# Optimization experiments

Measured on AMD Instinct MI355X. Metric: run time of the kernel, lower is better.

The kernel has to match this reference:

```python
import jax, jax.numpy as jnp
import numpy as np

NUM_NODES = 1_000_000
EMBED_DIM = 128
BATCH = 16384
K = 32  # max neighbors per node (padded)


def setup_inputs() -> dict:
    key = jax.random.key(0)
    k1, k2, k3, k4, k5, k6 = jax.random.split(key, 6)
    node_parameters = jax.random.normal(k1, (NUM_NODES, EMBED_DIM), dtype=jnp.float32) * 0.1
    node_indices = jax.random.randint(k2, (BATCH,), 0, NUM_NODES)
    pos_idx = jax.random.randint(k3, (BATCH, K), 0, NUM_NODES)
    pos_len = jax.random.randint(k4, (BATCH,), 0, K + 1)
    neg_idx = jax.random.randint(k5, (BATCH, K), 0, NUM_NODES)
    neg_len = jax.random.randint(k6, (BATCH,), 0, K + 1)
    return {
        "node_parameters": node_parameters,
        "node_indices": node_indices,
        "pos_idx": pos_idx,
        "pos_len": pos_len,
        "neg_idx": neg_idx,
        "neg_len": neg_len,
    }


def _masked_mean(table, idx, length):
    # table: [N, D], idx: [B, K], length: [B] -> [B, D]
    gathered = table[idx]  # [B, K, D]
    mask = (jnp.arange(idx.shape[1])[None, :] < length[:, None]).astype(table.dtype)  # [B, K]
    summed = jnp.einsum("bkd,bk->bd", gathered, mask)
    denom = length.astype(table.dtype)
    inv = jnp.where(denom > 0, 1.0 / jnp.maximum(denom, 1.0), 0.0)  # empty list -> zeros
    return summed * inv[:, None]


def reference(node_parameters, node_indices, pos_idx, pos_len, neg_idx, neg_len):
    node_embeds = node_parameters[node_indices]  # [B, D]
    pos_embeds = _masked_mean(node_parameters, pos_idx, pos_len)  # [B, D]
    neg_embeds = _masked_mean(node_parameters, neg_idx, neg_len)  # [B, D]
    return node_embeds, pos_embeds, neg_embeds
```

## Files before the change

### kernel.cpp

```cpp
#include <hip/hip_runtime.h>


constexpr int B = 16384;
constexpr int K = 32;

__global__ __launch_bounds__(256) void isne_kernel(
    const float* __restrict__ table,
    const int*   __restrict__ node_idx,
    const int*   __restrict__ pos_idx,
    const int*   __restrict__ pos_len,
    const int*   __restrict__ neg_idx,
    const int*   __restrict__ neg_len,
    float*       __restrict__ out)
{
    const int b     = blockIdx.x;
    const int tid   = threadIdx.x;
    const int side  = tid >> 7;
    const int stid  = tid & 127;
    const int grp   = stid >> 5;
    const int lane4 = stid & 31;
    const int sub   = stid >> 6;
    const int kbase = grp * 8;

    const float4* t4   = reinterpret_cast<const float4*>(table);
    float4*       out4 = reinterpret_cast<float4*>(out);

    if (tid < 32) {
        const int ni = node_idx[b];
        out4[(size_t)b * 32 + tid] = t4[(size_t)ni * 32 + tid];
    }

    const int* idxp = side ? neg_idx : pos_idx;
    const int  len  = (side ? neg_len : pos_len)[b];

    int ridx[8];
#pragma unroll
    for (int j = 0; j < 8; ++j) {
        const int k  = kbase + j;
        const int kk = (k < len) ? k : 0;
        ridx[j] = idxp[b * K + kk];
    }

    float4 v[8];
#pragma unroll
    for (int j = 0; j < 8; ++j) {
        v[j] = t4[(size_t)ridx[j] * 32 + lane4];
    }

    float4 acc = make_float4(0.f, 0.f, 0.f, 0.f);
#pragma unroll
    for (int j = 0; j < 8; ++j) {
        const float w = ((kbase + j) < len) ? 1.0f : 0.0f;
        acc.x += v[j].x * w;
        acc.y += v[j].y * w;
        acc.z += v[j].z * w;
        acc.w += v[j].w * w;
    }

    acc.x += __shfl_xor(acc.x, 32);
    acc.y += __shfl_xor(acc.y, 32);
    acc.z += __shfl_xor(acc.z, 32);
    acc.w += __shfl_xor(acc.w, 32);

    __shared__ float4 smem[2][32];
    if (sub == 1 && (stid & 63) < 32) smem[side][lane4] = acc;
    __syncthreads();
    if (sub == 0 && stid < 32) {
        float4 o = smem[side][lane4];
        o.x += acc.x; o.y += acc.y; o.z += acc.z; o.w += acc.w;
        const float inv = (len > 0) ? (1.0f / (float)len) : 0.0f;
        o.x *= inv; o.y *= inv; o.z *= inv; o.w *= inv;
        out4[((size_t)(1 + side) * B + b) * 32 + lane4] = o;
    }
}

extern "C" void kernel_launch(void* const* d_in, const int* in_sizes, int n_in,
                              void* d_out, int out_size, void* d_ws, size_t ws_size,
                              hipStream_t stream)
{
    const float* table    = (const float*)d_in[0];
    const int*   node_idx = (const int*)d_in[1];
    const int*   pos_idx  = (const int*)d_in[2];
    const int*   pos_len  = (const int*)d_in[3];
    const int*   neg_idx  = (const int*)d_in[4];
    const int*   neg_len  = (const int*)d_in[5];
    float*       out      = (float*)d_out;

    isne_kernel<<<B, 256, 0, stream>>>(table, node_idx, pos_idx, pos_len,
                                       neg_idx, neg_len, out);
}
```

Baseline: 609.3 us.

## Map one wave per batch row and side, skip gathers beyond list length

Restructures the kernel so each 64-lane wave handles one (batch row, pos/neg side) pair and reads each 512-byte row as float2 per lane. Neighbor indices are loaded once per wave and broadcast with readlane, and chunks of 8 neighbors past the list length are skipped entirely. This removes the shared-memory cross-wave reduction and the __syncthreads, and avoids fetching padded rows that the mask would zero out. In exchange each lane issues narrower loads and the wave works through the neighbors serially rather than splitting them across threads.

```diff
diff --git a/kernel.cpp b/kernel.cpp
--- a/kernel.cpp
+++ b/kernel.cpp
@@ -13,65 +13,54 @@
     const int*   __restrict__ neg_len,
     float*       __restrict__ out)
 {
-    const int b     = blockIdx.x;
-    const int tid   = threadIdx.x;
-    const int side  = tid >> 7;
-    const int stid  = tid & 127;
-    const int grp   = stid >> 5;
-    const int lane4 = stid & 31;
-    const int sub   = stid >> 6;
-    const int kbase = grp * 8;
+    const int tid  = threadIdx.x;
+    const int wave = tid >> 6;
+    const int lane = tid & 63;
+    const int b    = blockIdx.x * 2 + (wave >> 1);
+    const int side = wave & 1;
 
-    const float4* t4   = reinterpret_cast<const float4*>(table);
-    float4*       out4 = reinterpret_cast<float4*>(out);
+    const float2* t2   = reinterpret_cast<const float2*>(table);
+    float2*       out2 = reinterpret_cast<float2*>(out);
 
-    if (tid < 32) {
-        const int ni = node_idx[b];
-        out4[(size_t)b * 32 + tid] = t4[(size_t)ni * 32 + tid];
+    if (side == 0) {
+        const int ni = __builtin_amdgcn_readfirstlane(node_idx[b]);
+        out2[(size_t)b * 64 + lane] = t2[(size_t)ni * 64 + lane];
     }
 
-    const int* idxp = side ? neg_idx : pos_idx;
-    const int  len  = (side ? neg_len : pos_len)[b];
+    const int* idxp = (side ? neg_idx : pos_idx) + b * K;
+    const int  len  = __builtin_amdgcn_readfirstlane((side ? neg_len : pos_len)[b]);
 
-    int ridx[8];
+    const int myidx = idxp[lane & 31];
+    const int sidx0 = __builtin_amdgcn_readlane(myidx, 0);
+
+    float2 acc = make_float2(0.f, 0.f);
+
 #pragma unroll
-    for (int j = 0; j < 8; ++j) {
-        const int k  = kbase + j;
-        const int kk = (k < len) ? k : 0;
-        ridx[j] = idxp[b * K + kk];
+    for (int c = 0; c < 4; ++c) {
+        const int base = c * 8;
+        if (len > base) {
+            float2 v[8];
+#pragma unroll
+            for (int j = 0; j < 8; ++j) {
+                const int k = base + j;
+                int sidx = __builtin_amdgcn_readlane(myidx, base + j);
+                sidx = (k < len) ? sidx : sidx0;
+                v[j] = t2[(size_t)sidx * 64 + lane];
+            }
+#pragma unroll
+            for (int j = 0; j < 8; ++j) {
+                const float w = ((base + j) < len) ? 1.0f : 0.0f;
+                acc.x += v[j].x * w;
+                acc.y += v[j].y * w;
+            }
+        }
     }
 
-    float4 v[8];
-#pragma unroll
-    for (int j = 0; j < 8; ++j) {
-        v[j] = t4[(size_t)ridx[j] * 32 + lane4];
-    }
+    const float inv = (len > 0) ? (1.0f / (float)len) : 0.0f;
+    acc.x *= inv;
+    acc.y *= inv;
 
-    float4 acc = make_float4(0.f, 0.f, 0.f, 0.f);
-#pragma unroll
-    for (int j = 0; j < 8; ++j) {
-        const float w = ((kbase + j) < len) ? 1.0f : 0.0f;
-        acc.x += v[j].x * w;
-        acc.y += v[j].y * w;
-        acc.z += v[j].z * w;
-        acc.w += v[j].w * w;
-    }
-
-    acc.x += __shfl_xor(acc.x, 32);
-    acc.y += __shfl_xor(acc.y, 32);
-    acc.z += __shfl_xor(acc.z, 32);
-    acc.w += __shfl_xor(acc.w, 32);
-
-    __shared__ float4 smem[2][32];
-    if (sub == 1 && (stid & 63) < 32) smem[side][lane4] = acc;
-    __syncthreads();
-    if (sub == 0 && stid < 32) {
-        float4 o = smem[side][lane4];
-        o.x += acc.x; o.y += acc.y; o.z += acc.z; o.w += acc.w;
-        const float inv = (len > 0) ? (1.0f / (float)len) : 0.0f;
-        o.x *= inv; o.y *= inv; o.z *= inv; o.w *= inv;
-        out4[((size_t)(1 + side) * B + b) * 32 + lane4] = o;
-    }
+    out2[((size_t)(1 + side) * B + b) * 64 + lane] = acc;
 }
 
 extern "C" void kernel_launch(void* const* d_in, const int* in_sizes, int n_in,
@@ -86,6 +75,6 @@
     const int*   neg_len  = (const int*)d_in[5];
     float*       out      = (float*)d_out;
 
-    isne_kernel<<<B, 256, 0, stream>>>(table, node_idx, pos_idx, pos_len,
-                                       neg_idx, neg_len, out);
+    isne_kernel<<<B / 2, 256, 0, stream>>>(table, node_idx, pos_idx, pos_len,
+                                           neg_idx, neg_len, out);
 }
```

Result: no change. 611.2 us (+0.3%).
